# Performance work log

Measured on AMD Instinct MI355X. Metric: run time of the kernel, lower is better.

Reference implementation:

```python
import jax, jax.numpy as jnp
import numpy as np

IN_F = 1024
OUT_F = 1024
GRID_SIZE = 5
SPLINE_ORDER = 3
GRID_RANGE = (-1.0, 1.0)


def _make_grid():
    h = (GRID_RANGE[1] - GRID_RANGE[0]) / GRID_SIZE
    g = jnp.arange(-SPLINE_ORDER, GRID_SIZE + SPLINE_ORDER + 1, dtype=jnp.float32) * h + GRID_RANGE[0]
    return jnp.broadcast_to(g, (IN_F, g.shape[0]))  # (F, grid_size + 2*order + 1)


def setup_inputs() -> dict:
    key = jax.random.key(0)
    k1, k2, k3, k4 = jax.random.split(key, 4)
    B = 8192
    x = jax.random.normal(k1, (B, IN_F), dtype=jnp.float32)
    base_weight = jax.random.normal(k2, (OUT_F, IN_F), dtype=jnp.float32) / np.sqrt(IN_F)
    # mimic reset_parameters: uniform noise scaled by scale_noise/grid_size
    spline_weight = (jax.random.uniform(k3, (OUT_F, IN_F, GRID_SIZE + SPLINE_ORDER)) - 0.5) * (0.1 / GRID_SIZE)
    spline_scaler = jax.random.normal(k4, (OUT_F, IN_F), dtype=jnp.float32) / np.sqrt(IN_F)
    grid = _make_grid()
    return {"x": x, "base_weight": base_weight, "spline_weight": spline_weight,
            "spline_scaler": spline_scaler, "grid": grid}


def b_splines(x, grid):
    # x: (B, F); grid: (F, G) with G = grid_size + 2*order + 1
    xe = x[:, :, None]  # (B, F, 1)
    bases = ((xe >= grid[:, :-1]) & (xe < grid[:, 1:])).astype(x.dtype)  # (B, F, G-1)
    for k in range(1, SPLINE_ORDER + 1):
        left = (xe - grid[:, : -(k + 1)]) / (grid[:, k:-1] - grid[:, : -(k + 1)])
        right = (grid[:, k + 1 :] - xe) / (grid[:, k + 1 :] - grid[:, 1:-k])
        bases = left * bases[:, :, :-1] + right * bases[:, :, 1:]
    return bases  # (B, F, grid_size + order)


def reference(x, base_weight, spline_weight, spline_scaler, grid):
    base_out = jax.nn.silu(x) @ base_weight.T  # (B, O)
    basis = b_splines(x, grid)  # (B, F, C)
    scaled_w = spline_weight * spline_scaler[:, :, None]  # (O, F, C)
    spline_out = jnp.einsum('bfc,ofc->bo', basis, scaled_w)
    return base_out + spline_out
```

## Files before the change

### kernel.cpp

```cpp
#include <hip/hip_runtime.h>
#include <hip/hip_bf16.h>

#define IN_F   1024
#define OUT_F  1024
#define NCH    9
#define KDIM   9216
#define BATCH  8192

#define BM 256
#define BN 256
#define BK 64
#define KHALF 4608
#define NTK (KHALF / BK)
#define TSZ 16384

typedef __attribute__((ext_vector_type(4))) float  f32x4;
typedef __attribute__((ext_vector_type(8))) __bf16 bf16x8;

typedef __attribute__((address_space(3))) unsigned short       lds_u16;
typedef const __attribute__((address_space(1))) unsigned short glb_u16;

__device__ inline unsigned short f2bf(float f) {
    union { float f; unsigned int u; } v; v.f = f;
    unsigned int u = v.u;
    unsigned int r = (u + 0x7FFFu + ((u >> 16) & 1u)) >> 16;
    return (unsigned short)r;
}

__global__ void wgt_kernel(const float* __restrict__ bw,
                           const float* __restrict__ sw,
                           const float* __restrict__ sc,
                           unsigned short* __restrict__ W) {
    int idx = blockIdx.x * blockDim.x + threadIdx.x;
    if (idx >= OUT_F * IN_F) return;
    int o = idx >> 10, f = idx & 1023;
    float scale = sc[idx];
    const float4* swp = (const float4*)(sw + (size_t)idx * 8);
    float4 w0 = swp[0], w1 = swp[1];
    unsigned short* Wb = W + (size_t)o * KDIM + f;
    Wb[0 * 1024] = f2bf(w0.x * scale);
    Wb[1 * 1024] = f2bf(w0.y * scale);
    Wb[2 * 1024] = f2bf(w0.z * scale);
    Wb[3 * 1024] = f2bf(w0.w * scale);
    Wb[4 * 1024] = f2bf(w1.x * scale);
    Wb[5 * 1024] = f2bf(w1.y * scale);
    Wb[6 * 1024] = f2bf(w1.z * scale);
    Wb[7 * 1024] = f2bf(w1.w * scale);
    Wb[8 * 1024] = f2bf(bw[idx]);
}

__global__ void act_kernel(const float* __restrict__ x,
                           unsigned short* __restrict__ A) {
    int idx = blockIdx.x * blockDim.x + threadIdx.x;
    if (idx >= BATCH * 256) return;
    float4 xv = ((const float4*)x)[idx];
    float xs[4] = {xv.x, xv.y, xv.z, xv.w};

    unsigned short vals[4][9];
#pragma unroll
    for (int e = 0; e < 4; ++e) {
        float v  = xs[e];
        float s  = v / (1.0f + __expf(-v));

        float t  = (v + 2.2f) * 2.5f;
        float jf = floorf(t);
        int   j  = (int)jf;
        float u  = t - jf;
        float u2 = u * u, u3 = u2 * u;
        float p0 = u3 * (1.0f / 6.0f);
        float p1 = (-3.0f * u3 + 3.0f * u2 + 3.0f * u + 1.0f) * (1.0f / 6.0f);
        float p2 = (3.0f * u3 - 6.0f * u2 + 4.0f) * (1.0f / 6.0f);
        float om = 1.0f - u;
        float p3 = om * om * om * (1.0f / 6.0f);
        bool valid = (v >= -2.2f) && (v < 2.2f);

#pragma unroll
        for (int c = 0; c < 8; ++c) {
            int p = j - c;
            float bv = 0.0f;
            if (valid)
                bv = (p == 0) ? p0 : (p == 1) ? p1 : (p == 2) ? p2 : (p == 3) ? p3 : 0.0f;
            vals[e][c] = f2bf(bv);
        }
        vals[e][8] = f2bf(s);
    }

    int r = idx >> 8, f4 = idx & 255;
    unsigned short* base = A + (size_t)r * KDIM + f4 * 4;
#pragma unroll
    for (int c = 0; c < 9; ++c) {
        uint2 pk;
        pk.x = (unsigned int)vals[0][c] | ((unsigned int)vals[1][c] << 16);
        pk.y = (unsigned int)vals[2][c] | ((unsigned int)vals[3][c] << 16);
        *(uint2*)(base + (size_t)c * 1024) = pk;
    }
}

#define DECLS(q) \
    const int ci##q = (q) * 512 + tid; \
    const int rr##q = ci##q >> 3; \
    const int sw##q = (((ci##q & 7) ^ (rr##q & 7)) << 3); \
    const unsigned short* srcA##q = Ap + (size_t)(m0 + rr##q) * KDIM + kbase + sw##q; \
    const unsigned short* srcB##q = Wp + (size_t)(n0 + rr##q) * KDIM + kbase + sw##q; \
    const int lo##q = ci##q << 3;

#define STAGE(q, pb) do { \
    __builtin_amdgcn_global_load_lds((glb_u16*)srcA##q, (lds_u16*)(lds + (pb) * TSZ) + lo##q, 16, 0, 0); \
    srcA##q += BK; \
    __builtin_amdgcn_global_load_lds((glb_u16*)srcB##q, (lds_u16*)(lds + 2 * TSZ + (pb) * TSZ) + lo##q, 16, 0, 0); \
    srcB##q += BK; \
} while (0)

#define RDA(buf, mi, kk) (*(const bf16x8*)&(buf)[(rowa + (mi) * 16) * BK + ((((kk) * 4 + lhi) ^ l7) << 3)])
#define RDB(buf, ni, kk) (*(const bf16x8*)&(buf)[(rowb + (ni) * 16) * BK + ((((kk) * 4 + lhi) ^ l7) << 3)])

#define MM1(ai, mi, ni) \
    acc[mi][ni] = __builtin_amdgcn_mfma_f32_16x16x32_bf16(a[ai][0], b[ni][0], acc[mi][ni], 0, 0, 0); \
    acc[mi][ni] = __builtin_amdgcn_mfma_f32_16x16x32_bf16(a[ai][1], b[ni][1], acc[mi][ni], 0, 0, 0);

#define MMQ(mh, nh) \
    MM1(0, (mh) * 4 + 0, (nh) * 2 + 0) MM1(0, (mh) * 4 + 0, (nh) * 2 + 1) \
    MM1(1, (mh) * 4 + 1, (nh) * 2 + 0) MM1(1, (mh) * 4 + 1, (nh) * 2 + 1) \
    MM1(2, (mh) * 4 + 2, (nh) * 2 + 0) MM1(2, (mh) * 4 + 2, (nh) * 2 + 1) \
    MM1(3, (mh) * 4 + 3, (nh) * 2 + 0) MM1(3, (mh) * 4 + 3, (nh) * 2 + 1)

#define TILE(pb, t) do { \
    const unsigned short* bufA = lds + (pb) * TSZ; \
    const unsigned short* bufB = lds + 2 * TSZ + (pb) * TSZ; \
    if ((t) + 1 < NTK) { STAGE(0, (pb) ^ 1); STAGE(1, (pb) ^ 1); STAGE(2, (pb) ^ 1); STAGE(3, (pb) ^ 1); } \
     \
    a[0][0] = RDA(bufA, 0, 0); a[0][1] = RDA(bufA, 0, 1); a[1][0] = RDA(bufA, 1, 0); a[1][1] = RDA(bufA, 1, 1); \
    a[2][0] = RDA(bufA, 2, 0); a[2][1] = RDA(bufA, 2, 1); a[3][0] = RDA(bufA, 3, 0); a[3][1] = RDA(bufA, 3, 1); \
    b[0][0] = RDB(bufB, 0, 0); b[0][1] = RDB(bufB, 0, 1); b[1][0] = RDB(bufB, 1, 0); b[1][1] = RDB(bufB, 1, 1); \
    __builtin_amdgcn_s_barrier(); \
    __builtin_amdgcn_s_setprio(1); MMQ(0, 0) __builtin_amdgcn_s_setprio(0); \
    __builtin_amdgcn_s_barrier(); \
     \
    b[2][0] = RDB(bufB, 2, 0); b[2][1] = RDB(bufB, 2, 1); b[3][0] = RDB(bufB, 3, 0); b[3][1] = RDB(bufB, 3, 1); \
    __builtin_amdgcn_s_barrier(); \
    __builtin_amdgcn_s_setprio(1); MMQ(0, 1) __builtin_amdgcn_s_setprio(0); \
    __builtin_amdgcn_s_barrier(); \
     \
    a[0][0] = RDA(bufA, 4, 0); a[0][1] = RDA(bufA, 4, 1); a[1][0] = RDA(bufA, 5, 0); a[1][1] = RDA(bufA, 5, 1); \
    a[2][0] = RDA(bufA, 6, 0); a[2][1] = RDA(bufA, 6, 1); a[3][0] = RDA(bufA, 7, 0); a[3][1] = RDA(bufA, 7, 1); \
    __builtin_amdgcn_s_barrier(); \
    __builtin_amdgcn_s_setprio(1); MMQ(1, 1) __builtin_amdgcn_s_setprio(0); \
    __builtin_amdgcn_s_barrier(); \
     \
    __builtin_amdgcn_s_setprio(1); MMQ(1, 0) __builtin_amdgcn_s_setprio(0); \
    asm volatile("s_waitcnt vmcnt(0)" ::: "memory"); \
    __builtin_amdgcn_s_barrier(); \
} while (0)

__global__ __launch_bounds__(512, 2) void gemm_ks(
    const unsigned short* __restrict__ Ap,
    const unsigned short* __restrict__ Wp,
    float* __restrict__ C, float* __restrict__ P, int mode) {
    __shared__ unsigned short lds[4 * TSZ];

    const int tid  = threadIdx.x;
    const int wave = tid >> 6;
    const int lane = tid & 63;
    const int lm16 = lane & 15;
    const int lhi  = lane >> 4;
    const int l7   = lane & 7;

    const int bid  = blockIdx.x;
    const int mg   = bid & 3;
    const int kb   = (bid >> 2) & 1;
    const int j    = bid >> 3;
    const int m0   = (mg * 8 + (j >> 2)) * BM;
    const int n0   = (j & 3) * BN;
    const int kbase = kb * KHALF;

    const int wr = wave >> 2;
    const int wc = wave & 3;
    const int rowa = wr * 128 + lm16;
    const int rowb = wc * 64 + lm16;

    f32x4 acc[8][4];
#pragma unroll
    for (int i = 0; i < 8; ++i)
#pragma unroll
        for (int jn = 0; jn < 4; ++jn) acc[i][jn] = (f32x4)(0.0f);

    DECLS(0) DECLS(1) DECLS(2) DECLS(3)

    STAGE(0, 0); STAGE(1, 0); STAGE(2, 0); STAGE(3, 0);
    asm volatile("s_waitcnt vmcnt(0)" ::: "memory");
    __builtin_amdgcn_s_barrier();

    bf16x8 a[4][2], b[4][2];
    for (int tt = 0; tt < NTK; tt += 2) {
        TILE(0, tt);
        TILE(1, tt + 1);
    }

    const int row0 = m0 + wr * 128 + (lhi << 2);
    const int col0 = n0 + wc * 64 + lm16;
    if (mode) {
#pragma unroll
        for (int mi = 0; mi < 8; ++mi)
#pragma unroll
            for (int ni = 0; ni < 4; ++ni)
#pragma unroll
                for (int r = 0; r < 4; ++r)
                    atomicAdd(&C[(size_t)(row0 + mi * 16 + r) * OUT_F + (col0 + ni * 16)], acc[mi][ni][r]);
    } else {
        float* dst = kb ? P : C;
#pragma unroll
        for (int mi = 0; mi < 8; ++mi)
#pragma unroll
            for (int ni = 0; ni < 4; ++ni)
#pragma unroll
                for (int r = 0; r < 4; ++r)
                    dst[(size_t)(row0 + mi * 16 + r) * OUT_F + (col0 + ni * 16)] = acc[mi][ni][r];
    }
}

__global__ void add_kernel(float* __restrict__ C, const float* __restrict__ P) {
    int i = blockIdx.x * blockDim.x + threadIdx.x;
    if (i >= BATCH * OUT_F / 4) return;
    f32x4* c4 = (f32x4*)C;
    const f32x4* p4 = (const f32x4*)P;
    c4[i] = c4[i] + p4[i];
}

extern "C" void kernel_launch(void* const* d_in, const int* in_sizes, int n_in,
                              void* d_out, int out_size, void* d_ws, size_t ws_size,
                              hipStream_t stream) {
    const float* x             = (const float*)d_in[0];
    const float* base_weight   = (const float*)d_in[1];
    const float* spline_weight = (const float*)d_in[2];
    const float* spline_scaler = (const float*)d_in[3];
    float* out = (float*)d_out;

    const size_t wbytes = (size_t)OUT_F * KDIM * 2;
    const size_t abytes = (size_t)BATCH * KDIM * 2;
    const size_t pbytes = (size_t)BATCH * OUT_F * 4;
    unsigned short* Wc   = (unsigned short*)d_ws;
    unsigned short* Abuf = (unsigned short*)((char*)d_ws + wbytes);
    float*          P    = (float*)((char*)d_ws + wbytes + abytes);

    const int mode = (ws_size >= wbytes + abytes + pbytes) ? 0 : 1;
    if (mode == 1)
        hipMemsetAsync(d_out, 0, pbytes, stream);

    wgt_kernel<<<(OUT_F * IN_F) / 256, 256, 0, stream>>>(
        base_weight, spline_weight, spline_scaler, Wc);
    act_kernel<<<(BATCH * 256) / 256, 256, 0, stream>>>(x, Abuf);

    gemm_ks<<<256, 512, 0, stream>>>(Abuf, Wc, out, P, mode);

    if (mode == 0)
        add_kernel<<<(BATCH * OUT_F / 4 + 255) / 256, 256, 0, stream>>>(out, P);
}
```

Measured before the change: 208.2 us.

## Replace double-buffered BK=64 GEMM loop with a four-slot BK=32 LDS ring

Halves the K-tile to 32 and replaces the two-buffer ping-pong with a four-slot LDS ring that keeps three tiles of async global-to-LDS loads in flight. vmcnt waits are tuned so each iteration only waits for the oldest stage. The XOR swizzle on the LDS layout is dropped in favour of a plain row-major tile. The aim is to hide global-load latency better, at the risk of LDS bank conflicts from the unswizzled layout and more barriers per unit of MFMA work.

```diff
diff --git a/kernel.cpp b/kernel.cpp
--- a/kernel.cpp
+++ b/kernel.cpp
@@ -9,10 +9,10 @@
 
 #define BM 256
 #define BN 256
-#define BK 64
+#define BK 32
 #define KHALF 4608
 #define NTK (KHALF / BK)
-#define TSZ 16384
+#define SLOT 16384
 
 typedef __attribute__((ext_vector_type(4))) float  f32x4;
 typedef __attribute__((ext_vector_type(8))) __bf16 bf16x8;
@@ -98,72 +98,39 @@
 
 #define DECLS(q) \
     const int ci##q = (q) * 512 + tid; \
-    const int rr##q = ci##q >> 3; \
-    const int sw##q = (((ci##q & 7) ^ (rr##q & 7)) << 3); \
-    const unsigned short* srcA##q = Ap + (size_t)(m0 + rr##q) * KDIM + kbase + sw##q; \
-    const unsigned short* srcB##q = Wp + (size_t)(n0 + rr##q) * KDIM + kbase + sw##q; \
-    const int lo##q = ci##q << 3;
-
-#define STAGE(q, pb) do { \
-    __builtin_amdgcn_global_load_lds((glb_u16*)srcA##q, (lds_u16*)(lds + (pb) * TSZ) + lo##q, 16, 0, 0); \
-    srcA##q += BK; \
-    __builtin_amdgcn_global_load_lds((glb_u16*)srcB##q, (lds_u16*)(lds + 2 * TSZ + (pb) * TSZ) + lo##q, 16, 0, 0); \
-    srcB##q += BK; \
-} while (0)
-
-#define RDA(buf, mi, kk) (*(const bf16x8*)&(buf)[(rowa + (mi) * 16) * BK + ((((kk) * 4 + lhi) ^ l7) << 3)])
-#define RDB(buf, ni, kk) (*(const bf16x8*)&(buf)[(rowb + (ni) * 16) * BK + ((((kk) * 4 + lhi) ^ l7) << 3)])
-
-#define MM1(ai, mi, ni) \
-    acc[mi][ni] = __builtin_amdgcn_mfma_f32_16x16x32_bf16(a[ai][0], b[ni][0], acc[mi][ni], 0, 0, 0); \
-    acc[mi][ni] = __builtin_amdgcn_mfma_f32_16x16x32_bf16(a[ai][1], b[ni][1], acc[mi][ni], 0, 0, 0);
-
-#define MMQ(mh, nh) \
-    MM1(0, (mh) * 4 + 0, (nh) * 2 + 0) MM1(0, (mh) * 4 + 0, (nh) * 2 + 1) \
-    MM1(1, (mh) * 4 + 1, (nh) * 2 + 0) MM1(1, (mh) * 4 + 1, (nh) * 2 + 1) \
-    MM1(2, (mh) * 4 + 2, (nh) * 2 + 0) MM1(2, (mh) * 4 + 2, (nh) * 2 + 1) \
-    MM1(3, (mh) * 4 + 3, (nh) * 2 + 0) MM1(3, (mh) * 4 + 3, (nh) * 2 + 1)
-
-#define TILE(pb, t) do { \
-    const unsigned short* bufA = lds + (pb) * TSZ; \
-    const unsigned short* bufB = lds + 2 * TSZ + (pb) * TSZ; \
-    if ((t) + 1 < NTK) { STAGE(0, (pb) ^ 1); STAGE(1, (pb) ^ 1); STAGE(2, (pb) ^ 1); STAGE(3, (pb) ^ 1); } \
-     \
-    a[0][0] = RDA(bufA, 0, 0); a[0][1] = RDA(bufA, 0, 1); a[1][0] = RDA(bufA, 1, 0); a[1][1] = RDA(bufA, 1, 1); \
-    a[2][0] = RDA(bufA, 2, 0); a[2][1] = RDA(bufA, 2, 1); a[3][0] = RDA(bufA, 3, 0); a[3][1] = RDA(bufA, 3, 1); \
-    b[0][0] = RDB(bufB, 0, 0); b[0][1] = RDB(bufB, 0, 1); b[1][0] = RDB(bufB, 1, 0); b[1][1] = RDB(bufB, 1, 1); \
-    __builtin_amdgcn_s_barrier(); \
-    __builtin_amdgcn_s_setprio(1); MMQ(0, 0) __builtin_amdgcn_s_setprio(0); \
-    __builtin_amdgcn_s_barrier(); \
-     \
-    b[2][0] = RDB(bufB, 2, 0); b[2][1] = RDB(bufB, 2, 1); b[3][0] = RDB(bufB, 3, 0); b[3][1] = RDB(bufB, 3, 1); \
-    __builtin_amdgcn_s_barrier(); \
-    __builtin_amdgcn_s_setprio(1); MMQ(0, 1) __builtin_amdgcn_s_setprio(0); \
-    __builtin_amdgcn_s_barrier(); \
-     \
-    a[0][0] = RDA(bufA, 4, 0); a[0][1] = RDA(bufA, 4, 1); a[1][0] = RDA(bufA, 5, 0); a[1][1] = RDA(bufA, 5, 1); \
-    a[2][0] = RDA(bufA, 6, 0); a[2][1] = RDA(bufA, 6, 1); a[3][0] = RDA(bufA, 7, 0); a[3][1] = RDA(bufA, 7, 1); \
-    __builtin_amdgcn_s_barrier(); \
-    __builtin_amdgcn_s_setprio(1); MMQ(1, 1) __builtin_amdgcn_s_setprio(0); \
-    __builtin_amdgcn_s_barrier(); \
-     \
-    __builtin_amdgcn_s_setprio(1); MMQ(1, 0) __builtin_amdgcn_s_setprio(0); \
-    asm volatile("s_waitcnt vmcnt(0)" ::: "memory"); \
-    __builtin_amdgcn_s_barrier(); \
-} while (0)
-
-__global__ __launch_bounds__(512, 2) void gemm_ks(
+    const int lo##q = ci##q << 3; \
+    const unsigned short* srcA##q = Ap + (size_t)(m0 + (ci##q >> 2)) * KDIM + kbase + ((ci##q & 3) << 3); \
+    const unsigned short* srcB##q = Wp + (size_t)(n0 + (ci##q >> 2)) * KDIM + kbase + ((ci##q & 3) << 3);
+
+#define STAGE_A(q, ns) do { \
+    __builtin_amdgcn_global_load_lds((glb_u16*)srcA##q, (lds_u16*)(ns) + lo##q, 16, 0, 0); \
+    srcA##q += BK; } while (0)
+
+#define STAGE_B(q, ns) do { \
+    __builtin_amdgcn_global_load_lds((glb_u16*)srcB##q, (lds_u16*)(ns) + 8192 + lo##q, 16, 0, 0); \
+    srcB##q += BK; } while (0)
+
+#define RDA(mi) (*(const bf16x8*)&sA[(rowa + (mi) * 16) * BK + koff])
+#define RDB(ni) (*(const bf16x8*)&sB[(rowb + (ni) * 16) * BK + koff])
+
+#define MM4(ai, mi) \
+    acc[mi][0] = __builtin_amdgcn_mfma_f32_16x16x32_bf16(a##ai, b0, acc[mi][0], 0, 0, 0); \
+    acc[mi][1] = __builtin_amdgcn_mfma_f32_16x16x32_bf16(a##ai, b1, acc[mi][1], 0, 0, 0); \
+    acc[mi][2] = __builtin_amdgcn_mfma_f32_16x16x32_bf16(a##ai, b2, acc[mi][2], 0, 0, 0); \
+    acc[mi][3] = __builtin_amdgcn_mfma_f32_16x16x32_bf16(a##ai, b3, acc[mi][3], 0, 0, 0);
+
+__global__ __launch_bounds__(512, 2) void gemm_ring(
     const unsigned short* __restrict__ Ap,
     const unsigned short* __restrict__ Wp,
     float* __restrict__ C, float* __restrict__ P, int mode) {
-    __shared__ unsigned short lds[4 * TSZ];
+    __shared__ unsigned short lds[4 * SLOT];
 
     const int tid  = threadIdx.x;
     const int wave = tid >> 6;
     const int lane = tid & 63;
     const int lm16 = lane & 15;
     const int lhi  = lane >> 4;
-    const int l7   = lane & 7;
+    const int koff = lhi << 3;
 
     const int bid  = blockIdx.x;
     const int mg   = bid & 3;
@@ -184,16 +151,50 @@
 #pragma unroll
         for (int jn = 0; jn < 4; ++jn) acc[i][jn] = (f32x4)(0.0f);
 
-    DECLS(0) DECLS(1) DECLS(2) DECLS(3)
-
-    STAGE(0, 0); STAGE(1, 0); STAGE(2, 0); STAGE(3, 0);
-    asm volatile("s_waitcnt vmcnt(0)" ::: "memory");
+    DECLS(0) DECLS(1)
+
+    {
+        unsigned short* ns = lds;
+        STAGE_A(0, ns); STAGE_A(1, ns); STAGE_B(0, ns); STAGE_B(1, ns);
+    }
+    {
+        unsigned short* ns = lds + SLOT;
+        STAGE_A(0, ns); STAGE_A(1, ns); STAGE_B(0, ns); STAGE_B(1, ns);
+    }
+    {
+        unsigned short* ns = lds + 2 * SLOT;
+        STAGE_A(0, ns); STAGE_A(1, ns); STAGE_B(0, ns); STAGE_B(1, ns);
+    }
+    asm volatile("s_waitcnt vmcnt(8)" ::: "memory");
     __builtin_amdgcn_s_barrier();
 
-    bf16x8 a[4][2], b[4][2];
-    for (int tt = 0; tt < NTK; tt += 2) {
-        TILE(0, tt);
-        TILE(1, tt + 1);
+#pragma unroll 4
+    for (int t = 0; t < NTK; ++t) {
+        const unsigned short* sA = lds + (t & 3) * SLOT;
+        const unsigned short* sB = sA + 8192;
+        unsigned short* ns = lds + ((t + 3) & 3) * SLOT;
+        const bool pf = (t + 3 < NTK);
+
+        if (pf) { STAGE_A(0, ns); STAGE_A(1, ns); }
+        bf16x8 a0 = RDA(0), a1 = RDA(1), a2 = RDA(2), a3 = RDA(3);
+        bf16x8 b0 = RDB(0), b1 = RDB(1), b2 = RDB(2), b3 = RDB(3);
+        __builtin_amdgcn_s_barrier();
+        __builtin_amdgcn_s_setprio(1);
+        MM4(0, 0) MM4(1, 1) MM4(2, 2) MM4(3, 3)
+        __builtin_amdgcn_s_setprio(0);
+        __builtin_amdgcn_s_barrier();
+
+        if (pf) { STAGE_B(0, ns); STAGE_B(1, ns); }
+        a0 = RDA(4); a1 = RDA(5); a2 = RDA(6); a3 = RDA(7);
+        __builtin_amdgcn_s_barrier();
+        __builtin_amdgcn_s_setprio(1);
+        MM4(0, 4) MM4(1, 5) MM4(2, 6) MM4(3, 7)
+        __builtin_amdgcn_s_setprio(0);
+
+        if (t <= NTK - 4)      asm volatile("s_waitcnt vmcnt(8)" ::: "memory");
+        else if (t == NTK - 3) asm volatile("s_waitcnt vmcnt(4)" ::: "memory");
+        else                   asm volatile("s_waitcnt vmcnt(0)" ::: "memory");
+        __builtin_amdgcn_s_barrier();
     }
 
     const int row0 = m0 + wr * 128 + (lhi << 2);
@@ -250,7 +251,7 @@
         base_weight, spline_weight, spline_scaler, Wc);
     act_kernel<<<(BATCH * 256) / 256, 256, 0, stream>>>(x, Abuf);
 
-    gemm_ks<<<256, 512, 0, stream>>>(Abuf, Wc, out, P, mode);
+    gemm_ring<<<256, 512, 0, stream>>>(Abuf, Wc, out, P, mode);
 
     if (mode == 0)
         add_kernel<<<(BATCH * OUT_F / 4 + 255) / 256, 256, 0, stream>>>(out, P);
```

Measured after the change: 214.2 us. +2.9%, slower.
